# Kernel tuning notes

Measured on AMD Instinct MI355X. Metric: run time of the kernel, lower is better.

The kernel has to match this reference:

```python
import jax, jax.numpy as jnp
import numpy as np

T, B, D_IN, D_H = 256, 256, 1024, 1024


def setup_inputs() -> dict:
    key = jax.random.key(0)
    k1, k2 = jax.random.split(key)
    seq = jax.random.normal(k1, (T, B, D_IN), dtype=jnp.float32)
    # Kaiming-ish init so tanh does not saturate
    W = jax.random.normal(k2, (D_H, D_IN + D_H), dtype=jnp.float32) / np.sqrt(D_IN + D_H)
    b = jnp.zeros((D_H,), dtype=jnp.float32)
    return {"seq": seq, "W": W, "b": b}


def reference(seq, W, b):
    # seq: (T, B, d_in); W: (d_h, d_in + d_h); b: (d_h,)
    d_h = W.shape[0]
    h0 = jnp.zeros((seq.shape[1], d_h), dtype=seq.dtype)

    def step(h, x):
        # h_{t+1} = tanh(W [h_t ; x_t] + b)
        h_new = jnp.tanh(jnp.concatenate([h, x], axis=-1) @ W.T + b)
        return h_new, h_new

    _, hs = jax.lax.scan(step, h0, seq)  # hs: (T, B, d_h)
    # Original returns the full hidden-state history including the initial zero state
    return jnp.concatenate([h0[None], hs], axis=0)  # (T+1, B, d_h)
```

## Files before the change

kernel.cpp:

```cpp
#include <hip/hip_runtime.h>

#define T_STEPS 256
#define BATCH   256
#define DIN     1024
#define DH      1024

typedef _Float16 half8_t __attribute__((ext_vector_type(8)));
typedef _Float16 half4_t __attribute__((ext_vector_type(4)));
typedef float    f32x4_t __attribute__((ext_vector_type(4)));

#define LDH  1032
#define REDW 68

#define CPOL_SYS 17

union H4U { half4_t h; unsigned long long u; };

__device__ __forceinline__ float ftanh(float x) {
    float t = x * 2.885390081777927f;
    float e = exp2f(t);
    float r = __builtin_amdgcn_rcpf(e + 1.0f);
    return 1.0f - 2.0f * r;
}

__global__ __launch_bounds__(256) void cvt_w(const float* __restrict__ W,
                                             _Float16* __restrict__ Wh,
                                             _Float16* __restrict__ Wx) {
    const int part = blockIdx.x >> 9;
    size_t base = ((size_t)(blockIdx.x & 511) * 256 + threadIdx.x) * 8;
    const int n = (int)(base >> 10);
    const int k = (int)(base & 1023);
    const float4* s = reinterpret_cast<const float4*>(W + (size_t)n * 2048 + part * 1024 + k);
    float4 a = s[0], b = s[1];
    half8_t h;
    h[0] = (_Float16)a.x; h[1] = (_Float16)a.y;
    h[2] = (_Float16)a.z; h[3] = (_Float16)a.w;
    h[4] = (_Float16)b.x; h[5] = (_Float16)b.y;
    h[6] = (_Float16)b.z; h[7] = (_Float16)b.w;
    _Float16* dst = part ? Wx : Wh;
    *reinterpret_cast<half8_t*>(dst + base) = h;
}

__global__ __launch_bounds__(256) void zero_h0(float* __restrict__ out,
                                               int* __restrict__ flags) {
    size_t i = (size_t)blockIdx.x * 256 + threadIdx.x;
    reinterpret_cast<float4*>(out)[i] = make_float4(0.f, 0.f, 0.f, 0.f);
    if (blockIdx.x == 0) {
#pragma unroll
        for (int j = 0; j < 16; ++j)
            __hip_atomic_store(&flags[(int)threadIdx.x * 16 + j], 0,
                               __ATOMIC_RELAXED, __HIP_MEMORY_SCOPE_SYSTEM);
    }
}

__global__ __launch_bounds__(256, 1) void rnn_fused(
        const _Float16* __restrict__ Wh,
        const _Float16* __restrict__ Wx,
        const float* __restrict__ bias,
        const float* __restrict__ seq,
        _Float16* __restrict__ Hh,
        int* __restrict__ flags,
        float* __restrict__ out) {
    __shared__ __align__(16) _Float16 hL[16 * LDH];
    __shared__ __align__(16) _Float16 xL[16 * LDH];
    __shared__ __align__(16) float redL[16 * REDW];

    const int tid  = threadIdx.x;
    const int m    = blockIdx.x & 15;
    const int n    = blockIdx.x >> 4;
    const int wave = tid >> 6;
    const int lane = tid & 63;
    const int fr   = lane & 15;
    const int quad = lane >> 4;

    half8_t wfrag[64];
    {
        const _Float16* wph = Wh + (size_t)(n * 64 + wave * 16 + fr) * DH + quad * 8;
        const _Float16* wpx = Wx + (size_t)(n * 64 + wave * 16 + fr) * DH + quad * 8;
#pragma unroll
        for (int ks = 0; ks < 32; ++ks) {
            wfrag[ks]      = *reinterpret_cast<const half8_t*>(wph + ks * 32);
            wfrag[32 + ks] = *reinterpret_cast<const half8_t*>(wpx + ks * 32);
        }
    }

    const int r  = tid >> 4;
    const int c4 = (tid & 15) * 4;
    const size_t orowg = (size_t)(m * 16 + r);
    int* myflag = flags + (m * 16 + n) * 16;

    const int xr = tid >> 4;
    const int xc = (tid & 15) * 4;
    const float* xbase = seq + ((size_t)m * 16 + xr) * DH + xc;

    const float4 bv4 = *reinterpret_cast<const float4*>(bias + n * 64 + c4);

    {
        float4 xv[16];
        const float* p = xbase;
#pragma unroll
        for (int c = 0; c < 16; ++c)
            xv[c] = *reinterpret_cast<const float4*>(p + c * 64);
#pragma unroll
        for (int c = 0; c < 16; ++c) {
            half4_t h4;
            h4[0] = (_Float16)xv[c].x; h4[1] = (_Float16)xv[c].y;
            h4[2] = (_Float16)xv[c].z; h4[3] = (_Float16)xv[c].w;
            *reinterpret_cast<half4_t*>(&xL[xr * LDH + xc + c * 64]) = h4;
        }
        __syncthreads();

        f32x4_t acc0 = {0.f,0.f,0.f,0.f}, acc1 = {0.f,0.f,0.f,0.f};
        const _Float16* pax = &xL[fr * LDH + quad * 8];
#pragma unroll
        for (int ks = 0; ks < 16; ++ks) {
            half8_t a0 = *reinterpret_cast<const half8_t*>(pax + (2 * ks) * 32);
            half8_t a1 = *reinterpret_cast<const half8_t*>(pax + (2 * ks + 1) * 32);
            acc0 = __builtin_amdgcn_mfma_f32_16x16x32_f16(a0, wfrag[32 + 2 * ks],     acc0, 0, 0, 0);
            acc1 = __builtin_amdgcn_mfma_f32_16x16x32_f16(a1, wfrag[32 + 2 * ks + 1], acc1, 0, 0, 0);
        }
        f32x4_t sum = acc0 + acc1;
#pragma unroll
        for (int q = 0; q < 4; ++q)
            redL[(quad * 4 + q) * REDW + wave * 16 + fr] = sum[q];
        __syncthreads();

        f32x4_t t4 = *reinterpret_cast<const f32x4_t*>(&redL[r * REDW + c4]);
        float4 v = make_float4(ftanh(t4[0] + bv4.x), ftanh(t4[1] + bv4.y),
                               ftanh(t4[2] + bv4.z), ftanh(t4[3] + bv4.w));
        *reinterpret_cast<float4*>(
            out + ((size_t)BATCH + orowg) * DH + n * 64 + c4) = v;
        H4U cv;
        cv.h[0] = (_Float16)v.x; cv.h[1] = (_Float16)v.y;
        cv.h[2] = (_Float16)v.z; cv.h[3] = (_Float16)v.w;
        __hip_atomic_store(
            (unsigned long long*)(Hh + ((size_t)BATCH + orowg) * DH + n * 64 + c4),
            cv.u, __ATOMIC_RELAXED, __HIP_MEMORY_SCOPE_SYSTEM);
        __syncthreads();
        if (tid == 0)
            __hip_atomic_store(myflag, 1, __ATOMIC_RELAXED, __HIP_MEMORY_SCOPE_SYSTEM);
    }

    for (int s = 1; s < T_STEPS; ++s) {
        float4 xv[16];
        const float* p = xbase + (size_t)s * (BATCH * DH);
#pragma unroll
        for (int c = 0; c < 16; ++c)
            xv[c] = *reinterpret_cast<const float4*>(p + c * 64);

        if (tid < 16) {
            const int* f = flags + (m * 16 + tid) * 16;
            int guard = 0;
            while (__hip_atomic_load(f, __ATOMIC_RELAXED, __HIP_MEMORY_SCOPE_SYSTEM) < s) {
                if (++guard > (1 << 24)) break;
            }
        }
        __syncthreads();

        const _Float16* hsrc = Hh + ((size_t)(s & 1) * BATCH + (size_t)m * 16) * DH;
#pragma unroll
        for (int i = 0; i < 8; ++i) {
            const int c   = wave * 8 + i;
            const int row = c >> 1;
            const int hf  = c & 1;
            const _Float16* src = hsrc + (size_t)row * DH + hf * 512 + lane * 8;
            __builtin_amdgcn_global_load_lds(
                (const __attribute__((address_space(1))) void*)src,
                (__attribute__((address_space(3))) void*)&hL[row * LDH + hf * 512],
                16, 0, CPOL_SYS);
        }
#pragma unroll
        for (int c = 0; c < 16; ++c) {
            half4_t h4;
            h4[0] = (_Float16)xv[c].x; h4[1] = (_Float16)xv[c].y;
            h4[2] = (_Float16)xv[c].z; h4[3] = (_Float16)xv[c].w;
            *reinterpret_cast<half4_t*>(&xL[xr * LDH + xc + c * 64]) = h4;
        }
        __syncthreads();

        f32x4_t acc0 = {0.f,0.f,0.f,0.f}, acc1 = {0.f,0.f,0.f,0.f};
        const _Float16* pah = &hL[fr * LDH + quad * 8];
        const _Float16* pax = &xL[fr * LDH + quad * 8];
#pragma unroll
        for (int ks = 0; ks < 16; ++ks) {
            half8_t a0 = *reinterpret_cast<const half8_t*>(pah + (2 * ks) * 32);
            half8_t a1 = *reinterpret_cast<const half8_t*>(pah + (2 * ks + 1) * 32);
            acc0 = __builtin_amdgcn_mfma_f32_16x16x32_f16(a0, wfrag[2 * ks],     acc0, 0, 0, 0);
            acc1 = __builtin_amdgcn_mfma_f32_16x16x32_f16(a1, wfrag[2 * ks + 1], acc1, 0, 0, 0);
        }
#pragma unroll
        for (int ks = 0; ks < 16; ++ks) {
            half8_t a0 = *reinterpret_cast<const half8_t*>(pax + (2 * ks) * 32);
            half8_t a1 = *reinterpret_cast<const half8_t*>(pax + (2 * ks + 1) * 32);
            acc0 = __builtin_amdgcn_mfma_f32_16x16x32_f16(a0, wfrag[32 + 2 * ks],     acc0, 0, 0, 0);
            acc1 = __builtin_amdgcn_mfma_f32_16x16x32_f16(a1, wfrag[32 + 2 * ks + 1], acc1, 0, 0, 0);
        }
        f32x4_t sum = acc0 + acc1;

#pragma unroll
        for (int q = 0; q < 4; ++q)
            redL[(quad * 4 + q) * REDW + wave * 16 + fr] = sum[q];
        __syncthreads();

        f32x4_t t4 = *reinterpret_cast<const f32x4_t*>(&redL[r * REDW + c4]);
        float4 v = make_float4(ftanh(t4[0] + bv4.x), ftanh(t4[1] + bv4.y),
                               ftanh(t4[2] + bv4.z), ftanh(t4[3] + bv4.w));
        *reinterpret_cast<float4*>(
            out + ((size_t)(s + 1) * BATCH + orowg) * DH + n * 64 + c4) = v;
        H4U cv;
        cv.h[0] = (_Float16)v.x; cv.h[1] = (_Float16)v.y;
        cv.h[2] = (_Float16)v.z; cv.h[3] = (_Float16)v.w;
        __hip_atomic_store(
            (unsigned long long*)(Hh + ((size_t)((s + 1) & 1) * BATCH + orowg) * DH
                                  + n * 64 + c4),
            cv.u, __ATOMIC_RELAXED, __HIP_MEMORY_SCOPE_SYSTEM);

        __syncthreads();
        if (tid == 0)
            __hip_atomic_store(myflag, s + 1, __ATOMIC_RELAXED, __HIP_MEMORY_SCOPE_SYSTEM);
    }
}

extern "C" void kernel_launch(void* const* d_in, const int* in_sizes, int n_in,
                              void* d_out, int out_size, void* d_ws, size_t ws_size,
                              hipStream_t stream) {
    const float* seq  = (const float*)d_in[0];
    const float* W    = (const float*)d_in[1];
    const float* bias = (const float*)d_in[2];
    float* out        = (float*)d_out;
    _Float16* Wh      = (_Float16*)d_ws;
    _Float16* Wx      = (_Float16*)d_ws + 1024 * 1024;
    _Float16* Hh      = (_Float16*)d_ws + 2 * 1024 * 1024;
    int* flags        = (int*)((char*)d_ws + 5 * 1024 * 1024);

    hipLaunchKernelGGL(cvt_w, dim3(1024), dim3(256), 0, stream, W, Wh, Wx);
    hipLaunchKernelGGL(zero_h0, dim3(256), dim3(256), 0, stream, out, flags);
    hipLaunchKernelGGL(rnn_fused, dim3(256), dim3(256), 0, stream,
                       Wh, Wx, bias, seq, Hh, flags, out);
}
```

Baseline: 1.351 ms.

## Specialize waves for hidden and input GEMMs and prefetch next-step input projection

The kernel moves from a 16x16 tiling to 32x32 tiles per block (8 row groups by 32 column groups) using 32x32x16 MFMA. Two waves handle the recurrent h·Wh half of K while the other two waves compute the x·Wx projection for the next step, ahead of time, into a double-buffered reduction area. This takes the input GEMM and its loads off the serial dependency chain between steps. The epilogue is split so one wave publishes the fp16 hidden state and flag while another writes the fp32 output. The risks are uneven wave load, fewer flags to poll per block but larger tiles, and the hidden-state path now running on only two waves.

```diff
diff --git a/kernel.cpp b/kernel.cpp
--- a/kernel.cpp
+++ b/kernel.cpp
@@ -5,12 +5,10 @@
 #define DIN     1024
 #define DH      1024
 
-typedef _Float16 half8_t __attribute__((ext_vector_type(8)));
-typedef _Float16 half4_t __attribute__((ext_vector_type(4)));
-typedef float    f32x4_t __attribute__((ext_vector_type(4)));
-
-#define LDH  1032
-#define REDW 68
+typedef _Float16 half8_t  __attribute__((ext_vector_type(8)));
+typedef _Float16 half4_t  __attribute__((ext_vector_type(4)));
+typedef float    f32x4_t  __attribute__((ext_vector_type(4)));
+typedef float    f32x16_t __attribute__((ext_vector_type(16)));
 
 #define CPOL_SYS 17
 
@@ -61,163 +59,162 @@
         _Float16* __restrict__ Hh,
         int* __restrict__ flags,
         float* __restrict__ out) {
-    __shared__ __align__(16) _Float16 hL[16 * LDH];
-    __shared__ __align__(16) _Float16 xL[16 * LDH];
-    __shared__ __align__(16) float redL[16 * REDW];
+    __shared__ __align__(16) _Float16 hL[2][32][520];
+    __shared__ __align__(16) float    redL[2][4][32][36];
 
     const int tid  = threadIdx.x;
-    const int m    = blockIdx.x & 15;
-    const int n    = blockIdx.x >> 4;
+    const int m    = blockIdx.x & 7;
+    const int n    = blockIdx.x >> 3;
     const int wave = tid >> 6;
     const int lane = tid & 63;
-    const int fr   = lane & 15;
-    const int quad = lane >> 4;
-
-    half8_t wfrag[64];
+    const int l31  = lane & 31;
+    const int lhi  = lane >> 5;
+    const bool hwave = (wave < 2);
+    const int k0 = (wave & 1) * 512;
+
+    half8_t wfrag[32];
     {
-        const _Float16* wph = Wh + (size_t)(n * 64 + wave * 16 + fr) * DH + quad * 8;
-        const _Float16* wpx = Wx + (size_t)(n * 64 + wave * 16 + fr) * DH + quad * 8;
-#pragma unroll
-        for (int ks = 0; ks < 32; ++ks) {
-            wfrag[ks]      = *reinterpret_cast<const half8_t*>(wph + ks * 32);
-            wfrag[32 + ks] = *reinterpret_cast<const half8_t*>(wpx + ks * 32);
-        }
-    }
-
-    const int r  = tid >> 4;
-    const int c4 = (tid & 15) * 4;
-    const size_t orowg = (size_t)(m * 16 + r);
-    int* myflag = flags + (m * 16 + n) * 16;
-
-    const int xr = tid >> 4;
-    const int xc = (tid & 15) * 4;
-    const float* xbase = seq + ((size_t)m * 16 + xr) * DH + xc;
-
-    const float4 bv4 = *reinterpret_cast<const float4*>(bias + n * 64 + c4);
-
-    {
-        float4 xv[16];
-        const float* p = xbase;
-#pragma unroll
-        for (int c = 0; c < 16; ++c)
-            xv[c] = *reinterpret_cast<const float4*>(p + c * 64);
-#pragma unroll
-        for (int c = 0; c < 16; ++c) {
-            half4_t h4;
-            h4[0] = (_Float16)xv[c].x; h4[1] = (_Float16)xv[c].y;
-            h4[2] = (_Float16)xv[c].z; h4[3] = (_Float16)xv[c].w;
-            *reinterpret_cast<half4_t*>(&xL[xr * LDH + xc + c * 64]) = h4;
+        const _Float16* Wsel = hwave ? Wh : Wx;
+        const _Float16* wp = Wsel + (size_t)(n * 32 + l31) * DH + k0 + lhi * 8;
+#pragma unroll
+        for (int ks = 0; ks < 32; ++ks)
+            wfrag[ks] = *reinterpret_cast<const half8_t*>(wp + ks * 16);
+    }
+
+    const int er = lane >> 1;
+    const int ec = (lane & 1) * 16;
+    f32x4_t bias4[4];
+#pragma unroll
+    for (int j = 0; j < 4; ++j)
+        bias4[j] = *reinterpret_cast<const f32x4_t*>(bias + n * 32 + ec + 4 * j);
+
+    int* myflag = flags + (m * 32 + n) * 16;
+
+    auto xpart = [&](int s, int buf) {
+        const float* xb = seq + ((size_t)s * BATCH + m * 32 + l31) * DIN
+                              + k0 + lhi * 8;
+        f32x16_t a0, a1;
+#pragma unroll
+        for (int i = 0; i < 16; ++i) { a0[i] = 0.f; a1[i] = 0.f; }
+#pragma unroll
+        for (int ks = 0; ks < 32; ks += 2) {
+            float4 f0 = *reinterpret_cast<const float4*>(xb + ks * 16);
+            float4 f1 = *reinterpret_cast<const float4*>(xb + ks * 16 + 4);
+            float4 g0 = *reinterpret_cast<const float4*>(xb + (ks + 1) * 16);
+            float4 g1 = *reinterpret_cast<const float4*>(xb + (ks + 1) * 16 + 4);
+            half8_t ha, hb;
+            ha[0] = (_Float16)f0.x; ha[1] = (_Float16)f0.y;
+            ha[2] = (_Float16)f0.z; ha[3] = (_Float16)f0.w;
+            ha[4] = (_Float16)f1.x; ha[5] = (_Float16)f1.y;
+            ha[6] = (_Float16)f1.z; ha[7] = (_Float16)f1.w;
+            hb[0] = (_Float16)g0.x; hb[1] = (_Float16)g0.y;
+            hb[2] = (_Float16)g0.z; hb[3] = (_Float16)g0.w;
+            hb[4] = (_Float16)g1.x; hb[5] = (_Float16)g1.y;
+            hb[6] = (_Float16)g1.z; hb[7] = (_Float16)g1.w;
+            a0 = __builtin_amdgcn_mfma_f32_32x32x16_f16(ha, wfrag[ks],     a0, 0, 0, 0);
+            a1 = __builtin_amdgcn_mfma_f32_32x32x16_f16(hb, wfrag[ks + 1], a1, 0, 0, 0);
+        }
+#pragma unroll
+        for (int reg = 0; reg < 16; ++reg) {
+            const int row = (reg & 3) + 8 * (reg >> 2) + 4 * lhi;
+            redL[buf][wave][row][l31] = a0[reg] + a1[reg];
+        }
+    };
+
+    auto epilogue = [&](int s, int buf) {
+        f32x4_t v[4];
+#pragma unroll
+        for (int j = 0; j < 4; ++j) {
+            f32x4_t t = *reinterpret_cast<const f32x4_t*>(&redL[buf][0][er][ec + 4 * j]);
+#pragma unroll
+            for (int w = 1; w < 4; ++w) {
+                f32x4_t p = *reinterpret_cast<const f32x4_t*>(&redL[buf][w][er][ec + 4 * j]);
+                t[0] += p[0]; t[1] += p[1]; t[2] += p[2]; t[3] += p[3];
+            }
+            v[j][0] = ftanh(t[0] + bias4[j][0]);
+            v[j][1] = ftanh(t[1] + bias4[j][1]);
+            v[j][2] = ftanh(t[2] + bias4[j][2]);
+            v[j][3] = ftanh(t[3] + bias4[j][3]);
+        }
+        if (wave == 0) {
+            _Float16* hp = Hh + ((size_t)((s + 1) & 1) * BATCH + m * 32 + er) * DH
+                              + n * 32 + ec;
+#pragma unroll
+            for (int j = 0; j < 4; ++j) {
+                H4U cv;
+                cv.h[0] = (_Float16)v[j][0]; cv.h[1] = (_Float16)v[j][1];
+                cv.h[2] = (_Float16)v[j][2]; cv.h[3] = (_Float16)v[j][3];
+                __hip_atomic_store((unsigned long long*)(hp + 4 * j), cv.u,
+                                   __ATOMIC_RELAXED, __HIP_MEMORY_SCOPE_SYSTEM);
+            }
+            asm volatile("s_waitcnt vmcnt(0)" ::: "memory");
+            if (tid == 0)
+                __hip_atomic_store(myflag, s + 1, __ATOMIC_RELAXED,
+                                   __HIP_MEMORY_SCOPE_SYSTEM);
+        } else {
+            float* op = out + ((size_t)(s + 1) * BATCH + m * 32 + er) * DH
+                            + n * 32 + ec;
+#pragma unroll
+            for (int j = 0; j < 4; ++j)
+                *reinterpret_cast<float4*>(op + 4 * j) =
+                    make_float4(v[j][0], v[j][1], v[j][2], v[j][3]);
+        }
+    };
+
+    if (hwave) {
+#pragma unroll
+        for (int reg = 0; reg < 16; ++reg) {
+            const int row = (reg & 3) + 8 * (reg >> 2) + 4 * lhi;
+            redL[0][wave][row][l31] = 0.f;
+        }
+    } else {
+        xpart(0, 0);
+    }
+    __syncthreads();
+    if (hwave) epilogue(0, 0);
+    else       xpart(1, 1);
+
+    for (int s = 1; s < T_STEPS; ++s) {
+        const int buf = s & 1;
+        if (hwave) {
+            const int* f = flags + (m * 32 + l31) * 16;
+            int guard = 0;
+            while (__hip_atomic_load(f, __ATOMIC_RELAXED,
+                                     __HIP_MEMORY_SCOPE_SYSTEM) < s) {
+                if (++guard > (1 << 24)) break;
+            }
+            const _Float16* hs = Hh + ((size_t)(s & 1) * BATCH + m * 32) * DH
+                                    + k0 + lane * 8;
+#pragma unroll
+            for (int r = 0; r < 32; ++r) {
+                __builtin_amdgcn_global_load_lds(
+                    (const __attribute__((address_space(1))) void*)(hs + (size_t)r * DH),
+                    (__attribute__((address_space(3))) void*)&hL[wave][r][0],
+                    16, 0, CPOL_SYS);
+            }
+            asm volatile("s_waitcnt vmcnt(0)" ::: "memory");
+
+            f32x16_t a0, a1;
+#pragma unroll
+            for (int i = 0; i < 16; ++i) { a0[i] = 0.f; a1[i] = 0.f; }
+#pragma unroll
+            for (int ks = 0; ks < 32; ks += 2) {
+                half8_t ha = *reinterpret_cast<const half8_t*>(
+                    &hL[wave][l31][ks * 16 + lhi * 8]);
+                half8_t hb = *reinterpret_cast<const half8_t*>(
+                    &hL[wave][l31][(ks + 1) * 16 + lhi * 8]);
+                a0 = __builtin_amdgcn_mfma_f32_32x32x16_f16(ha, wfrag[ks],     a0, 0, 0, 0);
+                a1 = __builtin_amdgcn_mfma_f32_32x32x16_f16(hb, wfrag[ks + 1], a1, 0, 0, 0);
+            }
+#pragma unroll
+            for (int reg = 0; reg < 16; ++reg) {
+                const int row = (reg & 3) + 8 * (reg >> 2) + 4 * lhi;
+                redL[buf][wave][row][l31] = a0[reg] + a1[reg];
+            }
         }
         __syncthreads();
-
-        f32x4_t acc0 = {0.f,0.f,0.f,0.f}, acc1 = {0.f,0.f,0.f,0.f};
-        const _Float16* pax = &xL[fr * LDH + quad * 8];
-#pragma unroll
-        for (int ks = 0; ks < 16; ++ks) {
-            half8_t a0 = *reinterpret_cast<const half8_t*>(pax + (2 * ks) * 32);
-            half8_t a1 = *reinterpret_cast<const half8_t*>(pax + (2 * ks + 1) * 32);
-            acc0 = __builtin_amdgcn_mfma_f32_16x16x32_f16(a0, wfrag[32 + 2 * ks],     acc0, 0, 0, 0);
-            acc1 = __builtin_amdgcn_mfma_f32_16x16x32_f16(a1, wfrag[32 + 2 * ks + 1], acc1, 0, 0, 0);
-        }
-        f32x4_t sum = acc0 + acc1;
-#pragma unroll
-        for (int q = 0; q < 4; ++q)
-            redL[(quad * 4 + q) * REDW + wave * 16 + fr] = sum[q];
-        __syncthreads();
-
-        f32x4_t t4 = *reinterpret_cast<const f32x4_t*>(&redL[r * REDW + c4]);
-        float4 v = make_float4(ftanh(t4[0] + bv4.x), ftanh(t4[1] + bv4.y),
-                               ftanh(t4[2] + bv4.z), ftanh(t4[3] + bv4.w));
-        *reinterpret_cast<float4*>(
-            out + ((size_t)BATCH + orowg) * DH + n * 64 + c4) = v;
-        H4U cv;
-        cv.h[0] = (_Float16)v.x; cv.h[1] = (_Float16)v.y;
-        cv.h[2] = (_Float16)v.z; cv.h[3] = (_Float16)v.w;
-        __hip_atomic_store(
-            (unsigned long long*)(Hh + ((size_t)BATCH + orowg) * DH + n * 64 + c4),
-            cv.u, __ATOMIC_RELAXED, __HIP_MEMORY_SCOPE_SYSTEM);
-        __syncthreads();
-        if (tid == 0)
-            __hip_atomic_store(myflag, 1, __ATOMIC_RELAXED, __HIP_MEMORY_SCOPE_SYSTEM);
-    }
-
-    for (int s = 1; s < T_STEPS; ++s) {
-        float4 xv[16];
-        const float* p = xbase + (size_t)s * (BATCH * DH);
-#pragma unroll
-        for (int c = 0; c < 16; ++c)
-            xv[c] = *reinterpret_cast<const float4*>(p + c * 64);
-
-        if (tid < 16) {
-            const int* f = flags + (m * 16 + tid) * 16;
-            int guard = 0;
-            while (__hip_atomic_load(f, __ATOMIC_RELAXED, __HIP_MEMORY_SCOPE_SYSTEM) < s) {
-                if (++guard > (1 << 24)) break;
-            }
-        }
-        __syncthreads();
-
-        const _Float16* hsrc = Hh + ((size_t)(s & 1) * BATCH + (size_t)m * 16) * DH;
-#pragma unroll
-        for (int i = 0; i < 8; ++i) {
-            const int c   = wave * 8 + i;
-            const int row = c >> 1;
-            const int hf  = c & 1;
-            const _Float16* src = hsrc + (size_t)row * DH + hf * 512 + lane * 8;
-            __builtin_amdgcn_global_load_lds(
-                (const __attribute__((address_space(1))) void*)src,
-                (__attribute__((address_space(3))) void*)&hL[row * LDH + hf * 512],
-                16, 0, CPOL_SYS);
-        }
-#pragma unroll
-        for (int c = 0; c < 16; ++c) {
-            half4_t h4;
-            h4[0] = (_Float16)xv[c].x; h4[1] = (_Float16)xv[c].y;
-            h4[2] = (_Float16)xv[c].z; h4[3] = (_Float16)xv[c].w;
-            *reinterpret_cast<half4_t*>(&xL[xr * LDH + xc + c * 64]) = h4;
-        }
-        __syncthreads();
-
-        f32x4_t acc0 = {0.f,0.f,0.f,0.f}, acc1 = {0.f,0.f,0.f,0.f};
-        const _Float16* pah = &hL[fr * LDH + quad * 8];
-        const _Float16* pax = &xL[fr * LDH + quad * 8];
-#pragma unroll
-        for (int ks = 0; ks < 16; ++ks) {
-            half8_t a0 = *reinterpret_cast<const half8_t*>(pah + (2 * ks) * 32);
-            half8_t a1 = *reinterpret_cast<const half8_t*>(pah + (2 * ks + 1) * 32);
-            acc0 = __builtin_amdgcn_mfma_f32_16x16x32_f16(a0, wfrag[2 * ks],     acc0, 0, 0, 0);
-            acc1 = __builtin_amdgcn_mfma_f32_16x16x32_f16(a1, wfrag[2 * ks + 1], acc1, 0, 0, 0);
-        }
-#pragma unroll
-        for (int ks = 0; ks < 16; ++ks) {
-            half8_t a0 = *reinterpret_cast<const half8_t*>(pax + (2 * ks) * 32);
-            half8_t a1 = *reinterpret_cast<const half8_t*>(pax + (2 * ks + 1) * 32);
-            acc0 = __builtin_amdgcn_mfma_f32_16x16x32_f16(a0, wfrag[32 + 2 * ks],     acc0, 0, 0, 0);
-            acc1 = __builtin_amdgcn_mfma_f32_16x16x32_f16(a1, wfrag[32 + 2 * ks + 1], acc1, 0, 0, 0);
-        }
-        f32x4_t sum = acc0 + acc1;
-
-#pragma unroll
-        for (int q = 0; q < 4; ++q)
-            redL[(quad * 4 + q) * REDW + wave * 16 + fr] = sum[q];
-        __syncthreads();
-
-        f32x4_t t4 = *reinterpret_cast<const f32x4_t*>(&redL[r * REDW + c4]);
-        float4 v = make_float4(ftanh(t4[0] + bv4.x), ftanh(t4[1] + bv4.y),
-                               ftanh(t4[2] + bv4.z), ftanh(t4[3] + bv4.w));
-        *reinterpret_cast<float4*>(
-            out + ((size_t)(s + 1) * BATCH + orowg) * DH + n * 64 + c4) = v;
-        H4U cv;
-        cv.h[0] = (_Float16)v.x; cv.h[1] = (_Float16)v.y;
-        cv.h[2] = (_Float16)v.z; cv.h[3] = (_Float16)v.w;
-        __hip_atomic_store(
-            (unsigned long long*)(Hh + ((size_t)((s + 1) & 1) * BATCH + orowg) * DH
-                                  + n * 64 + c4),
-            cv.u, __ATOMIC_RELAXED, __HIP_MEMORY_SCOPE_SYSTEM);
-
-        __syncthreads();
-        if (tid == 0)
-            __hip_atomic_store(myflag, s + 1, __ATOMIC_RELAXED, __HIP_MEMORY_SCOPE_SYSTEM);
+        if (hwave)        epilogue(s, buf);
+        else if (s < 255) xpart(s + 1, (s + 1) & 1);
     }
 }
 
```

Result: slower. 3.277 ms (+142.6%).

## Overlap input projection with flag wait and double-buffer x prefetch

Applied to the files above, without the earlier changes.

The x-part MFMA is computed before spinning on neighbour flags, and the next step's x is prefetched into a double-buffered LDS tile. This takes the input projection and x load latency off the serial recurrence path. The h load is split into two halves waited on with explicit vmcnt counts, so the first half of the h GEMM can start before the second half lands. The output store is moved after the flag publish, __syncthreads is replaced by raw barriers with manual waitcnt, and the flags are packed contiguously. The hand-written vmcnt counts and sched barriers are fragile and depend on the exact order of memory instructions the compiler emits.

```diff
diff --git a/kernel.cpp b/kernel.cpp
--- a/kernel.cpp
+++ b/kernel.cpp
@@ -15,6 +15,11 @@
 #define CPOL_SYS 17
 
 union H4U { half4_t h; unsigned long long u; };
+
+#define WAITVM(N)  asm volatile("s_waitcnt vmcnt(" #N ")" ::: "memory")
+#define WAITLGKM0  asm volatile("s_waitcnt lgkmcnt(0)" ::: "memory")
+#define RBAR()     do { __builtin_amdgcn_s_barrier(); \
+                        __builtin_amdgcn_sched_barrier(0); } while (0)
 
 __device__ __forceinline__ float ftanh(float x) {
     float t = x * 2.885390081777927f;
@@ -45,12 +50,9 @@
                                                int* __restrict__ flags) {
     size_t i = (size_t)blockIdx.x * 256 + threadIdx.x;
     reinterpret_cast<float4*>(out)[i] = make_float4(0.f, 0.f, 0.f, 0.f);
-    if (blockIdx.x == 0) {
-#pragma unroll
-        for (int j = 0; j < 16; ++j)
-            __hip_atomic_store(&flags[(int)threadIdx.x * 16 + j], 0,
-                               __ATOMIC_RELAXED, __HIP_MEMORY_SCOPE_SYSTEM);
-    }
+    if (blockIdx.x == 0)
+        __hip_atomic_store(&flags[(int)threadIdx.x], 0,
+                           __ATOMIC_RELAXED, __HIP_MEMORY_SCOPE_SYSTEM);
 }
 
 __global__ __launch_bounds__(256, 1) void rnn_fused(
@@ -62,7 +64,7 @@
         int* __restrict__ flags,
         float* __restrict__ out) {
     __shared__ __align__(16) _Float16 hL[16 * LDH];
-    __shared__ __align__(16) _Float16 xL[16 * LDH];
+    __shared__ __align__(16) _Float16 xL[2][16 * LDH];
     __shared__ __align__(16) float redL[16 * REDW];
 
     const int tid  = threadIdx.x;
@@ -87,7 +89,7 @@
     const int r  = tid >> 4;
     const int c4 = (tid & 15) * 4;
     const size_t orowg = (size_t)(m * 16 + r);
-    int* myflag = flags + (m * 16 + n) * 16;
+    int* myflag = flags + (m * 16 + n);
 
     const int xr = tid >> 4;
     const int xc = (tid & 15) * 4;
@@ -95,23 +97,23 @@
 
     const float4 bv4 = *reinterpret_cast<const float4*>(bias + n * 64 + c4);
 
+    float4 xv[16];
+
     {
-        float4 xv[16];
-        const float* p = xbase;
 #pragma unroll
         for (int c = 0; c < 16; ++c)
-            xv[c] = *reinterpret_cast<const float4*>(p + c * 64);
+            xv[c] = *reinterpret_cast<const float4*>(xbase + c * 64);
 #pragma unroll
         for (int c = 0; c < 16; ++c) {
             half4_t h4;
             h4[0] = (_Float16)xv[c].x; h4[1] = (_Float16)xv[c].y;
             h4[2] = (_Float16)xv[c].z; h4[3] = (_Float16)xv[c].w;
-            *reinterpret_cast<half4_t*>(&xL[xr * LDH + xc + c * 64]) = h4;
-        }
-        __syncthreads();
+            *reinterpret_cast<half4_t*>(&xL[0][xr * LDH + xc + c * 64]) = h4;
+        }
+        WAITLGKM0; RBAR();
 
         f32x4_t acc0 = {0.f,0.f,0.f,0.f}, acc1 = {0.f,0.f,0.f,0.f};
-        const _Float16* pax = &xL[fr * LDH + quad * 8];
+        const _Float16* pax = &xL[0][fr * LDH + quad * 8];
 #pragma unroll
         for (int ks = 0; ks < 16; ++ks) {
             half8_t a0 = *reinterpret_cast<const half8_t*>(pax + (2 * ks) * 32);
@@ -123,90 +125,115 @@
 #pragma unroll
         for (int q = 0; q < 4; ++q)
             redL[(quad * 4 + q) * REDW + wave * 16 + fr] = sum[q];
-        __syncthreads();
+        WAITLGKM0; RBAR();
 
         f32x4_t t4 = *reinterpret_cast<const f32x4_t*>(&redL[r * REDW + c4]);
         float4 v = make_float4(ftanh(t4[0] + bv4.x), ftanh(t4[1] + bv4.y),
                                ftanh(t4[2] + bv4.z), ftanh(t4[3] + bv4.w));
-        *reinterpret_cast<float4*>(
-            out + ((size_t)BATCH + orowg) * DH + n * 64 + c4) = v;
         H4U cv;
         cv.h[0] = (_Float16)v.x; cv.h[1] = (_Float16)v.y;
         cv.h[2] = (_Float16)v.z; cv.h[3] = (_Float16)v.w;
         __hip_atomic_store(
             (unsigned long long*)(Hh + ((size_t)BATCH + orowg) * DH + n * 64 + c4),
             cv.u, __ATOMIC_RELAXED, __HIP_MEMORY_SCOPE_SYSTEM);
-        __syncthreads();
+        WAITVM(0); RBAR();
         if (tid == 0)
             __hip_atomic_store(myflag, 1, __ATOMIC_RELAXED, __HIP_MEMORY_SCOPE_SYSTEM);
-    }
-
-    for (int s = 1; s < T_STEPS; ++s) {
-        float4 xv[16];
-        const float* p = xbase + (size_t)s * (BATCH * DH);
+
+        *reinterpret_cast<float4*>(
+            out + ((size_t)BATCH + orowg) * DH + n * 64 + c4) = v;
 #pragma unroll
         for (int c = 0; c < 16; ++c)
-            xv[c] = *reinterpret_cast<const float4*>(p + c * 64);
-
-        if (tid < 16) {
-            const int* f = flags + (m * 16 + tid) * 16;
-            int guard = 0;
-            while (__hip_atomic_load(f, __ATOMIC_RELAXED, __HIP_MEMORY_SCOPE_SYSTEM) < s) {
-                if (++guard > (1 << 24)) break;
-            }
-        }
-        __syncthreads();
-
-        const _Float16* hsrc = Hh + ((size_t)(s & 1) * BATCH + (size_t)m * 16) * DH;
-#pragma unroll
-        for (int i = 0; i < 8; ++i) {
-            const int c   = wave * 8 + i;
-            const int row = c >> 1;
-            const int hf  = c & 1;
-            const _Float16* src = hsrc + (size_t)row * DH + hf * 512 + lane * 8;
-            __builtin_amdgcn_global_load_lds(
-                (const __attribute__((address_space(1))) void*)src,
-                (__attribute__((address_space(3))) void*)&hL[row * LDH + hf * 512],
-                16, 0, CPOL_SYS);
-        }
+            xv[c] = *reinterpret_cast<const float4*>(
+                xbase + (size_t)BATCH * DH + c * 64);
 #pragma unroll
         for (int c = 0; c < 16; ++c) {
             half4_t h4;
             h4[0] = (_Float16)xv[c].x; h4[1] = (_Float16)xv[c].y;
             h4[2] = (_Float16)xv[c].z; h4[3] = (_Float16)xv[c].w;
-            *reinterpret_cast<half4_t*>(&xL[xr * LDH + xc + c * 64]) = h4;
-        }
-        __syncthreads();
+            *reinterpret_cast<half4_t*>(&xL[1][xr * LDH + xc + c * 64]) = h4;
+        }
+        WAITLGKM0; RBAR();
+    }
+
+    for (int s = 1; s < T_STEPS; ++s) {
+        const int buf = s & 1;
 
         f32x4_t acc0 = {0.f,0.f,0.f,0.f}, acc1 = {0.f,0.f,0.f,0.f};
+        {
+            const _Float16* pax = &xL[buf][fr * LDH + quad * 8];
+#pragma unroll
+            for (int ks = 0; ks < 16; ++ks) {
+                half8_t a0 = *reinterpret_cast<const half8_t*>(pax + (2 * ks) * 32);
+                half8_t a1 = *reinterpret_cast<const half8_t*>(pax + (2 * ks + 1) * 32);
+                acc0 = __builtin_amdgcn_mfma_f32_16x16x32_f16(a0, wfrag[32 + 2 * ks],     acc0, 0, 0, 0);
+                acc1 = __builtin_amdgcn_mfma_f32_16x16x32_f16(a1, wfrag[32 + 2 * ks + 1], acc1, 0, 0, 0);
+            }
+        }
+
+        if (tid < 16) {
+            const int* f = flags + (m * 16 + tid);
+            int guard = 0;
+            while (__hip_atomic_load(f, __ATOMIC_RELAXED,
+                                     __HIP_MEMORY_SCOPE_SYSTEM) < s) {
+                if (++guard > (1 << 24)) break;
+            }
+        }
+        RBAR();
+
+        const _Float16* hsrc = Hh + ((size_t)buf * BATCH + (size_t)m * 16) * DH;
+#pragma unroll
+        for (int i = 0; i < 4; ++i) {
+            const int row = wave * 4 + i;
+            __builtin_amdgcn_global_load_lds(
+                (const __attribute__((address_space(1))) void*)(hsrc + (size_t)row * DH + lane * 8),
+                (__attribute__((address_space(3))) void*)&hL[row * LDH],
+                16, 0, CPOL_SYS);
+        }
+#pragma unroll
+        for (int i = 0; i < 4; ++i) {
+            const int row = wave * 4 + i;
+            __builtin_amdgcn_global_load_lds(
+                (const __attribute__((address_space(1))) void*)(hsrc + (size_t)row * DH + 512 + lane * 8),
+                (__attribute__((address_space(3))) void*)&hL[row * LDH + 512],
+                16, 0, CPOL_SYS);
+        }
+        {
+            const int sn = (s < 255) ? s + 1 : 255;
+            const float* p = xbase + (size_t)sn * (BATCH * DH);
+#pragma unroll
+            for (int c = 0; c < 16; ++c)
+                xv[c] = *reinterpret_cast<const float4*>(p + c * 64);
+        }
+
+        WAITVM(20);
+        RBAR();
         const _Float16* pah = &hL[fr * LDH + quad * 8];
-        const _Float16* pax = &xL[fr * LDH + quad * 8];
-#pragma unroll
-        for (int ks = 0; ks < 16; ++ks) {
+#pragma unroll
+        for (int ks = 0; ks < 8; ++ks) {
             half8_t a0 = *reinterpret_cast<const half8_t*>(pah + (2 * ks) * 32);
             half8_t a1 = *reinterpret_cast<const half8_t*>(pah + (2 * ks + 1) * 32);
             acc0 = __builtin_amdgcn_mfma_f32_16x16x32_f16(a0, wfrag[2 * ks],     acc0, 0, 0, 0);
             acc1 = __builtin_amdgcn_mfma_f32_16x16x32_f16(a1, wfrag[2 * ks + 1], acc1, 0, 0, 0);
         }
-#pragma unroll
-        for (int ks = 0; ks < 16; ++ks) {
-            half8_t a0 = *reinterpret_cast<const half8_t*>(pax + (2 * ks) * 32);
-            half8_t a1 = *reinterpret_cast<const half8_t*>(pax + (2 * ks + 1) * 32);
-            acc0 = __builtin_amdgcn_mfma_f32_16x16x32_f16(a0, wfrag[32 + 2 * ks],     acc0, 0, 0, 0);
-            acc1 = __builtin_amdgcn_mfma_f32_16x16x32_f16(a1, wfrag[32 + 2 * ks + 1], acc1, 0, 0, 0);
+        WAITVM(16);
+        RBAR();
+#pragma unroll
+        for (int ks = 8; ks < 16; ++ks) {
+            half8_t a0 = *reinterpret_cast<const half8_t*>(pah + (2 * ks) * 32);
+            half8_t a1 = *reinterpret_cast<const half8_t*>(pah + (2 * ks + 1) * 32);
+            acc0 = __builtin_amdgcn_mfma_f32_16x16x32_f16(a0, wfrag[2 * ks],     acc0, 0, 0, 0);
+            acc1 = __builtin_amdgcn_mfma_f32_16x16x32_f16(a1, wfrag[2 * ks + 1], acc1, 0, 0, 0);
         }
         f32x4_t sum = acc0 + acc1;
-
 #pragma unroll
         for (int q = 0; q < 4; ++q)
             redL[(quad * 4 + q) * REDW + wave * 16 + fr] = sum[q];
-        __syncthreads();
+        WAITLGKM0; RBAR();
 
         f32x4_t t4 = *reinterpret_cast<const f32x4_t*>(&redL[r * REDW + c4]);
         float4 v = make_float4(ftanh(t4[0] + bv4.x), ftanh(t4[1] + bv4.y),
                                ftanh(t4[2] + bv4.z), ftanh(t4[3] + bv4.w));
-        *reinterpret_cast<float4*>(
-            out + ((size_t)(s + 1) * BATCH + orowg) * DH + n * 64 + c4) = v;
         H4U cv;
         cv.h[0] = (_Float16)v.x; cv.h[1] = (_Float16)v.y;
         cv.h[2] = (_Float16)v.z; cv.h[3] = (_Float16)v.w;
@@ -214,10 +241,22 @@
             (unsigned long long*)(Hh + ((size_t)((s + 1) & 1) * BATCH + orowg) * DH
                                   + n * 64 + c4),
             cv.u, __ATOMIC_RELAXED, __HIP_MEMORY_SCOPE_SYSTEM);
-
-        __syncthreads();
+        WAITVM(0);
+        RBAR();
         if (tid == 0)
-            __hip_atomic_store(myflag, s + 1, __ATOMIC_RELAXED, __HIP_MEMORY_SCOPE_SYSTEM);
+            __hip_atomic_store(myflag, s + 1, __ATOMIC_RELAXED,
+                               __HIP_MEMORY_SCOPE_SYSTEM);
+
+        *reinterpret_cast<float4*>(
+            out + ((size_t)(s + 1) * BATCH + orowg) * DH + n * 64 + c4) = v;
+#pragma unroll
+        for (int c = 0; c < 16; ++c) {
+            half4_t h4;
+            h4[0] = (_Float16)xv[c].x; h4[1] = (_Float16)xv[c].y;
+            h4[2] = (_Float16)xv[c].z; h4[3] = (_Float16)xv[c].w;
+            *reinterpret_cast<half4_t*>(&xL[buf ^ 1][xr * LDH + xc + c * 64]) = h4;
+        }
+        WAITLGKM0; RBAR();
     }
 }
 
```

New measurement: 1.402 ms. +3.7%, slower.
